# Kernel optimization log

Hardware: AMD Instinct MI355X
Metric: run time of the kernel (lower is better)

Reference implementation:

```python
import jax, jax.numpy as jnp
import numpy as np

NEG_INF = -1e30  # safe -inf surrogate to avoid nan in logsumexp


def _ctc_loss_sum(log_probs, labels, input_lengths, label_lengths):
    # log_probs: (T, N, C) already log-softmaxed; blank = 0
    T, N, C = log_probs.shape
    S = labels.shape[1]
    L = 2 * S + 1  # extended label sequence: blank-interleaved

    # extended labels: [blank, y1, blank, y2, ..., blank]
    ext = jnp.zeros((N, L), dtype=jnp.int32).at[:, 1::2].set(labels.astype(jnp.int32))
    # gather emission log-probs for extended labels: (T, N, L)
    lp_ext = jnp.take_along_axis(log_probs, jnp.broadcast_to(ext[None], (T, N, L)), axis=2)

    # transition from l-2 allowed only for non-blank labels differing from ext[l-2]
    ext_m2 = jnp.pad(ext, ((0, 0), (2, 0)), constant_values=-1)[:, :L]
    allow_skip = (ext != 0) & (ext != ext_m2)  # (N, L)

    # alpha at t=0
    alpha0 = jnp.full((N, L), NEG_INF, dtype=log_probs.dtype)
    alpha0 = alpha0.at[:, 0].set(lp_ext[0, :, 0])
    alpha0 = alpha0.at[:, 1].set(jnp.where(label_lengths > 0, lp_ext[0, :, 1], NEG_INF))

    def step(alpha, t_and_lp):
        t, lp_t = t_and_lp  # lp_t: (N, L)
        a1 = jnp.pad(alpha, ((0, 0), (1, 0)), constant_values=NEG_INF)[:, :L]
        a2 = jnp.pad(alpha, ((0, 0), (2, 0)), constant_values=NEG_INF)[:, :L]
        a2 = jnp.where(allow_skip, a2, NEG_INF)
        m = jnp.maximum(jnp.maximum(alpha, a1), a2)
        lse = m + jnp.log(jnp.exp(alpha - m) + jnp.exp(a1 - m) + jnp.exp(a2 - m))
        new = jnp.where(m > NEG_INF / 2, lse + lp_t, NEG_INF)
        # freeze alpha past each sequence's input length
        alpha = jnp.where((t < input_lengths)[:, None], new, alpha)
        return alpha, None

    alpha, _ = jax.lax.scan(step, alpha0, (jnp.arange(1, T), lp_ext[1:]))

    # log-likelihood = logsumexp(alpha[2*Sl], alpha[2*Sl - 1])
    idx = (2 * label_lengths).astype(jnp.int32)
    a_last = jnp.take_along_axis(alpha, idx[:, None], axis=1)[:, 0]
    a_prev = jnp.take_along_axis(alpha, jnp.maximum(idx - 1, 0)[:, None], axis=1)[:, 0]
    a_prev = jnp.where(label_lengths > 0, a_prev, NEG_INF)
    m = jnp.maximum(a_last, a_prev)
    ll = m + jnp.log(jnp.exp(a_last - m) + jnp.exp(a_prev - m))
    loss = -ll
    # zero_infinity=True: replace infinite losses with 0
    loss = jnp.where(loss < -NEG_INF / 2, loss, 0.0)
    return jnp.sum(loss)


def setup_inputs() -> dict:
    T, N, C, S = 512, 32, 4000, 64
    key = jax.random.key(0)
    k1, k2 = jax.random.split(key)
    inputs = jax.random.normal(k1, (T, N, C), dtype=jnp.float32)
    labels = jax.random.randint(k2, (N, S), 1, C, dtype=jnp.int32)  # exclude blank=0
    input_lengths = jnp.full((N,), T, dtype=jnp.int32)
    label_lengths = jnp.full((N,), S, dtype=jnp.int32)
    return {"inputs": inputs, "labels": labels,
            "input_lengths": input_lengths, "label_lengths": label_lengths}


def reference(inputs, labels, input_lengths, label_lengths):
    log_probs = jax.nn.log_softmax(inputs, axis=2)
    return _ctc_loss_sum(log_probs, labels, input_lengths, label_lengths)
```

## Files before the change

kernel.cpp:

```cpp
#include <hip/hip_runtime.h>

#define LN2 0.6931471805599453f

constexpr int T = 512, N = 32, C = 4000, S = 64;
constexpr int TN   = T * N;
constexpr int ROWF = 68;
constexpr int CT   = 16;
constexpr int NCF  = 16;
constexpr int NCB  = 16;
constexpr int NCG  = 32;

__global__ __launch_bounds__(256) void k_softmax_probs(
    const float* __restrict__ x, const int* __restrict__ labels,
    float* __restrict__ pp, float* __restrict__ ee)
{
    int row  = blockIdx.x * 4 + (threadIdx.x >> 6);
    int lane = threadIdx.x & 63;
    const float*  rp  = x + (size_t)row * C;
    const float4* rp4 = reinterpret_cast<const float4*>(rp);

    float m = -INFINITY, s = 0.f;
    #pragma unroll
    for (int k = 0; k < 15; ++k) {
        float4 v = rp4[lane + 64 * k];
        float mv = fmaxf(fmaxf(v.x, v.y), fmaxf(v.z, v.w));
        float s4 = __expf(v.x - mv) + __expf(v.y - mv) +
                   __expf(v.z - mv) + __expf(v.w - mv);
        float nm = fmaxf(m, mv);
        s = s * __expf(m - nm) + s4 * __expf(mv - nm);
        m = nm;
    }
    if (lane < 40) {
        float4 v = rp4[960 + lane];
        float mv = fmaxf(fmaxf(v.x, v.y), fmaxf(v.z, v.w));
        float s4 = __expf(v.x - mv) + __expf(v.y - mv) +
                   __expf(v.z - mv) + __expf(v.w - mv);
        float nm = fmaxf(m, mv);
        s = s * __expf(m - nm) + s4 * __expf(mv - nm);
        m = nm;
    }
    for (int off = 32; off; off >>= 1) {
        float om = __shfl_xor(m, off), os = __shfl_xor(s, off);
        float nm = fmaxf(m, om);
        s = s * __expf(m - nm) + os * __expf(om - nm);
        m = nm;
    }
    float logZ = m + __logf(s);

    int t = row >> 5, n = row & 31;
    int c  = labels[n * S + lane];
    float zb = rp[0];
    float zl = rp[c];

    float wm = zl;
    for (int off = 32; off; off >>= 1) wm = fmaxf(wm, __shfl_xor(wm, off));
    wm = fmaxf(wm, zb);
    float pm = __expf(wm - logZ);
    int e = (int)(__float_as_uint(pm) >> 23) - 127;

    float* outp = pp + ((size_t)n * T + t) * ROWF;
    outp[1 + lane] = ldexpf(__expf(zl - logZ), -e);
    if (lane == 0) {
        outp[0] = ldexpf(__expf(zb - logZ), -e);
        ee[n * T + t] = (float)e;
    }
}

__device__ __forceinline__ float dpp_shr1_zero(float x) {
    int r = __builtin_amdgcn_update_dpp(0, __float_as_int(x),
                                        0x138 , 0xf, 0xf, false);
    return __int_as_float(r);
}
__device__ __forceinline__ float dpp_shl1_zero(float x) {
    int r = __builtin_amdgcn_update_dpp(0, __float_as_int(x),
                                        0x130 , 0xf, 0xf, false);
    return __int_as_float(r);
}
template <int CTRL>
__device__ __forceinline__ float dpp_max_step(float x) {
    int t = __builtin_amdgcn_update_dpp(__float_as_int(x), __float_as_int(x),
                                        CTRL, 0xf, 0xf, false);
    return fmaxf(x, __int_as_float(t));
}
__device__ __forceinline__ float wave_max_bcast(float x) {
    x = dpp_max_step<0xB1>(x);  x = dpp_max_step<0x4E>(x);
    x = dpp_max_step<0x141>(x); x = dpp_max_step<0x140>(x);
    x = dpp_max_step<0x142>(x); x = dpp_max_step<0x143>(x);
    return __int_as_float(__builtin_amdgcn_readlane(__float_as_int(x), 63));
}

__global__ __launch_bounds__(128) void k_ctc_alpha(
    const float* __restrict__ pp, const float* __restrict__ ee,
    const int* __restrict__ labels,
    const int* __restrict__ input_len, const int* __restrict__ label_len,
    float* __restrict__ out)
{
    __shared__ __align__(16) float ldsF[2][CT][ROWF];
    __shared__ __align__(16) float ldsB[2][CT][ROWF];
    __shared__ float gj[132];
    const int n = blockIdx.x;
    const int wid = threadIdx.x >> 6, lane = threadIdx.x & 63;
    const int Tin = input_len[n], Sl = label_len[n];
    const float* bp = pp + (size_t)n * T * ROWF;
    const bool hot = (Tin == T);

    const int li   = labels[n * S + lane];
    const int lim1 = lane ? labels[n * S + lane - 1] : -1;
    const float skf  = (lane > 0 && li != 0 && li != lim1) ? 1.f : 0.f;
    const float skUf = dpp_shr1_zero(skf);
    const float skk  = skf * skUf;
    const float skD  = dpp_shl1_zero(skf);

    asm volatile("s_waitcnt vmcnt(0)" ::: "memory");
    __builtin_amdgcn_sched_barrier(0);

    float a0 = 0.f, a1 = 0.f, aX = 0.f;
    int SH = 0;

#define ISSUE_F(cc) do {                                                      \
    const float* cp_ = bp + (size_t)(cc) * CT * ROWF;                         \
    if (lane < 17) {                                                          \
        _Pragma("unroll")                                                     \
        for (int d_ = 0; d_ < CT; ++d_)                                       \
            __builtin_amdgcn_global_load_lds(cp_ + (size_t)d_ * ROWF + lane * 4, \
                                             &ldsF[(cc) & 1][d_][0], 16, 0, 0);\
    } } while (0)
#define ISSUE_B(cc) do {                                                      \
    const float* cp_ = bp + (size_t)(496 - 16 * (cc)) * ROWF;                 \
    if (lane < 17) {                                                          \
        _Pragma("unroll")                                                     \
        for (int d_ = 0; d_ < CT; ++d_)                                       \
            __builtin_amdgcn_global_load_lds(cp_ + (size_t)d_ * ROWF + lane * 4, \
                                             &ldsB[(cc) & 1][d_][0], 16, 0, 0);\
    } } while (0)

#define PAIRS(B, D) do {                                                      \
    const float* R0_ = &ldsF[B][D][0];                                        \
    const float* R1_ = &ldsF[B][(D) + 1][0];                                  \
    float cb1 = R0_[0], cl1 = R0_[1 + lane];                                  \
    float cb2 = R1_[0], cl2 = R1_[1 + lane];                                  \
    float clU = dpp_shr1_zero(cl1);                                           \
    float W   = clU * cl2;                                                    \
    float A   = cb1 * cb2;                                                    \
    float B_  = clU * cb2;                                                    \
    float Cc  = A + B_;                                                       \
    float D_  = skUf * B_;                                                    \
    float s1  = cb1 + cl1;                                                    \
    float E   = s1 * cl2;                                                     \
    float F   = cl1 * cl2;                                                    \
    float G   = skf * W;                                                      \
    float H   = fmaf(skf, F + W, cb1 * cl2);                                  \
    float I   = skk * W;                                                      \
    float Y0  = cl1 * cb2;                                                    \
    float Y1  = s1 * cb2;                                                     \
    float Y2  = skf * Y0;                                                     \
    float p1  = dpp_shr1_zero(a1);                                            \
    float p0  = dpp_shr1_zero(a0);                                            \
    float p2  = dpp_shr1_zero(p1);                                            \
    float n0  = fmaf(p0, B_, a0 * A) + fmaf(p2, D_, p1 * Cc);                 \
    float n1  = fmaf(a1, F, a0 * E) + fmaf(p2, I, fmaf(p1, H, p0 * G));       \
    float nX  = fmaf(a1, Y1, aX * A) + fmaf(p1, Y2, a0 * Y0);                 \
    a0 = n0; a1 = n1; aX = nX;                                                \
} while (0)

#define WINDOW4(B, D0) do {                                                   \
    a0 = ldexpf(a0, kA); a1 = ldexpf(a1, kA); aX = ldexpf(aX, kA);            \
    SH += kA;                                                                 \
    float gnow_ = fmaxf(fmaxf(a0, a1), aX);                                   \
    PAIRS(B, D0);                                                             \
    gs = dpp_max_step<0xB1>(gs);  gs = dpp_max_step<0x4E>(gs);                \
    PAIRS(B, (D0) + 2);                                                       \
    gs = dpp_max_step<0x141>(gs); gs = dpp_max_step<0x140>(gs);               \
    PAIRS(B, (D0) + 4);                                                       \
    gs = dpp_max_step<0x142>(gs); gs = dpp_max_step<0x143>(gs);               \
    PAIRS(B, (D0) + 6);                                                       \
    {   unsigned b_ = (unsigned)__builtin_amdgcn_readlane(__float_as_int(gs), 63); \
        int e_ = (int)(b_ >> 23) - 127;                                       \
        kA = (b_ == 0u) ? 0 : (105 - e_ - kA);                                \
    }                                                                         \
    gs = gnow_;                                                               \
} while (0)

#define BSTEPT(B, D) do {                                                     \
    const float* R_ = &ldsB[B][D][0];                                         \
    float cb_ = R_[0], cl_ = R_[1 + lane];                                    \
    float cD_ = dpp_shl1_zero(cl_);                         \
    float d1_ = dpp_shl1_zero(g1);                           \
    float d0s_ = dpp_shl1_zero(g0);                          \
    float d0_ = (lane == 63) ? gX : d0s_;             \
    float cg_ = cl_ * g1;                                                     \
    float ng0 = fmaf(cb_, g0, cg_);                                           \
    float ng1 = fmaf(skD * cD_, d1_, fmaf(cb_, d0_, cg_));                    \
    float ngX = cb_ * gX;                                                     \
    g0 = ng0; g1 = ng1; gX = ngX;                                             \
} while (0)
#define BRENORM do {                                                          \
    float g_ = wave_max_bcast(fmaxf(g0, fmaxf(g1, gX)));                      \
    unsigned b_ = __float_as_uint(g_);                                        \
    int k_ = (b_ == 0u) ? 0 : (100 - ((int)(b_ >> 23) - 127));                \
    g0 = ldexpf(g0, k_); g1 = ldexpf(g1, k_); gX = ldexpf(gX, k_);            \
    SHb += k_;                                                                \
} while (0)

    if (wid == 0) {
        if (hot) {
            int kA = 0; float gs = 0.f;
            ISSUE_F(0); ISSUE_F(1);
            asm volatile("s_waitcnt vmcnt(16)" ::: "memory");
            __builtin_amdgcn_sched_barrier(0);
            a0 = (lane == 0) ? ldsF[0][0][0] : 0.f;
            a1 = (lane == 0 && Sl > 0) ? ldsF[0][0][1] : 0.f;
            {
                float cb = ldsF[0][1][0], cl = ldsF[0][1][1 + lane];
                float p1 = dpp_shr1_zero(a1);
                float n0 = (a0 + p1) * cb;
                float n1 = fmaf(skf, p1, a0 + a1) * cl;
                float nX = (aX + a1) * cb;
                a0 = n0; a1 = n1; aX = nX;
            }
            PAIRS(0, 2); PAIRS(0, 4); PAIRS(0, 6);
            {   float g = wave_max_bcast(fmaxf(fmaxf(a0, a1), aX));
                unsigned b = __float_as_uint(g);
                int k0 = (b == 0u) ? 0 : (105 - ((int)(b >> 23) - 127));
                a0 = ldexpf(a0, k0); a1 = ldexpf(a1, k0); aX = ldexpf(aX, k0);
                SH += k0; kA = 0;
                gs = fmaxf(fmaxf(a0, a1), aX);
            }
            WINDOW4(0, 8);
            __builtin_amdgcn_sched_barrier(0);
            ISSUE_F(2);
            for (int c = 1; c < NCF; ++c) {
                if (c < NCF - 1) { asm volatile("s_waitcnt vmcnt(16)" ::: "memory"); }
                else             { asm volatile("s_waitcnt vmcnt(0)"  ::: "memory"); }
                __builtin_amdgcn_sched_barrier(0);
                int buf = c & 1;
                WINDOW4(buf, 0);
                WINDOW4(buf, 8);
                if (c + 2 < NCF) {
                    __builtin_amdgcn_sched_barrier(0);
                    ISSUE_F(c + 2);
                }
            }
        } else {
#define GSTEP(cc, dd) do {                                                    \
    float cb_ = ldsF[(cc) & 1][dd][0];                                        \
    float cl_ = ldsF[(cc) & 1][dd][1 + lane];                                 \
    float p1_ = dpp_shr1_zero(a1);                                            \
    float na0_ = (a0 + p1_) * cb_;                                            \
    float na1_ = fmaf(skf, p1_, a0 + a1) * cl_;                               \
    float naX_ = (aX + a1) * cb_;                                             \
    int t_ = (cc) * CT + (dd);                                                \
    bool act_ = (unsigned)(t_ - 1) < (unsigned)(Tin - 1);                     \
    a0 = act_ ? na0_ : a0;                                                    \
    a1 = act_ ? na1_ : a1;                                                    \
    aX = act_ ? naX_ : aX;                                                    \
    if (((dd) & 3) == 3) {                                                    \
        float g_ = wave_max_bcast(fmaxf(a0, fmaxf(a1, aX)));                  \
        unsigned b_ = __float_as_uint(g_);                                    \
        int k_ = (b_ == 0u) ? 0 : (100 - ((int)(b_ >> 23) - 127));            \
        a0 = ldexpf(a0, k_); a1 = ldexpf(a1, k_); aX = ldexpf(aX, k_);        \
        SH += k_;                                                             \
    }                                                                         \
} while (0)
            ISSUE_F(0); ISSUE_F(1);
            asm volatile("s_waitcnt vmcnt(16)" ::: "memory");
            __builtin_amdgcn_sched_barrier(0);
            a0 = (lane == 0) ? ldsF[0][0][0] : 0.f;
            a1 = (lane == 0 && Sl > 0) ? ldsF[0][0][1] : 0.f;
            #pragma unroll
            for (int d = 1; d < CT; ++d) GSTEP(0, d);
            __builtin_amdgcn_sched_barrier(0);
            ISSUE_F(2);
            for (int c = 1; c < NCG; ++c) {
                if (c < NCG - 1) { asm volatile("s_waitcnt vmcnt(16)" ::: "memory"); }
                else             { asm volatile("s_waitcnt vmcnt(0)"  ::: "memory"); }
                __builtin_amdgcn_sched_barrier(0);
                #pragma unroll
                for (int d = 0; d < CT; ++d) GSTEP(c, d);
                if (c + 2 < NCG) {
                    __builtin_amdgcn_sched_barrier(0);
                    ISSUE_F(c + 2);
                }
            }
#undef GSTEP
        }
    } else if (hot) {
        float g0 = (lane == Sl) ? 1.f : 0.f;
        float g1 = (Sl > 0 && lane == Sl - 1) ? 1.f : 0.f;
        float gX = (Sl >= S && lane == 63) ? 1.f : 0.f;
        int SHb = 0;

        ISSUE_B(0); ISSUE_B(1);
        for (int c = 0; c < NCB; ++c) {
            if (c < NCB - 1) { asm volatile("s_waitcnt vmcnt(16)" ::: "memory"); }
            else             { asm volatile("s_waitcnt vmcnt(0)"  ::: "memory"); }
            __builtin_amdgcn_sched_barrier(0);
            int buf = c & 1;
            BSTEPT(buf, 15); BSTEPT(buf, 14); BSTEPT(buf, 13); BSTEPT(buf, 12);
            BRENORM;
            BSTEPT(buf, 11); BSTEPT(buf, 10); BSTEPT(buf, 9);  BSTEPT(buf, 8);
            BRENORM;
            BSTEPT(buf, 7);  BSTEPT(buf, 6);  BSTEPT(buf, 5);  BSTEPT(buf, 4);
            BRENORM;
            BSTEPT(buf, 3);  BSTEPT(buf, 2);  BSTEPT(buf, 1);  BSTEPT(buf, 0);
            BRENORM;
            if (c + 2 < NCB) {
                __builtin_amdgcn_sched_barrier(0);
                ISSUE_B(c + 2);
            }
        }
        gj[2 * lane]     = ldexpf(g0, -120);
        gj[2 * lane + 1] = ldexpf(g1, -120);
        if (lane == 63) {
            gj[128] = ldexpf(gX, -120);
            gj[130] = (float)SHb;
        }
    }

    __syncthreads();
    if (wid != 0) return;

    float se = 0.f;
    #pragma unroll
    for (int j = 0; j < 8; ++j) {
        int idx = lane + 64 * j;
        float ev = ee[n * T + idx];
        se += (idx < Tin) ? ev : 0.f;
    }
    for (int off = 32; off; off >>= 1) se += __shfl_xor(se, off);

    if (hot) {
        float term = a0 * gj[2 * lane] + a1 * gj[2 * lane + 1];
        if (lane == 63) term = fmaf(aX, gj[128], term);
        for (int off = 32; off; off >>= 1) term += __shfl_xor(term, off);
        if (lane == 0) {
            float SHb = gj[130];
            float ll2  = log2f(term) - (float)SH - SHb + 120.f + se;
            float loss = -ll2 * LN2;
            if (!(loss < 5e29f)) loss = 0.f;
            atomicAdd(out, loss);
        }
    } else {
        float a_last = (Sl >= S) ? __shfl(aX, 63) : __shfl(a0, Sl);
        float a_prev_raw = __shfl(a1, (Sl > 0) ? (Sl - 1) : 0);
        float a_prev = (Sl > 0) ? a_prev_raw : 0.f;
        if (lane == 0) {
            float sum  = a_last + a_prev;
            float ll2  = log2f(sum) - (float)SH + se;
            float loss = -ll2 * LN2;
            if (!(loss < 5e29f)) loss = 0.f;
            atomicAdd(out, loss);
        }
    }
#undef BRENORM
#undef BSTEPT
#undef WINDOW4
#undef PAIRS
#undef ISSUE_F
#undef ISSUE_B
}

extern "C" void kernel_launch(void* const* d_in, const int* in_sizes, int n_in,
                              void* d_out, int out_size, void* d_ws, size_t ws_size,
                              hipStream_t stream) {
    const float* x       = (const float*)d_in[0];
    const int*   labels  = (const int*)d_in[1];
    const int*   in_len  = (const int*)d_in[2];
    const int*   lab_len = (const int*)d_in[3];
    float* out  = (float*)d_out;
    float* pp   = (float*)d_ws;
    float* ee   = pp + (size_t)TN * ROWF + 256;

    hipMemsetAsync(out, 0, sizeof(float), stream);
    k_softmax_probs<<<TN / 4, 256, 0, stream>>>(x, labels, pp, ee);
    k_ctc_alpha<<<N, 128, 0, stream>>>(pp, ee, labels, in_len, lab_len, out);
}
```

Before: 81.55 us.

## Fuse backward CTC steps into two-step transfer and rebalance forward/backward chunks

The backward beta recursion now advances two timesteps per update by precomposing the two emission rows into a banded two-step transfer matrix. This halves the serial dependent DPP/FMA chain per step pair. The meeting point moves so the forward pass handles 8 chunks and the backward pass 24, balancing the now cheaper backward wave against the forward wave. The final combine switches to double precision and drops the fixed ldexp offset. The cost is more arithmetic per pair and changed rounding behaviour.

```diff
diff --git a/kernel.cpp b/kernel.cpp
--- a/kernel.cpp
+++ b/kernel.cpp
@@ -6,8 +6,8 @@
 constexpr int TN   = T * N;
 constexpr int ROWF = 68;
 constexpr int CT   = 16;
-constexpr int NCF  = 16;
-constexpr int NCB  = 16;
+constexpr int NCF  = 8;
+constexpr int NCB  = 24;
 constexpr int NCG  = 32;
 
 __global__ __launch_bounds__(256) void k_softmax_probs(
@@ -110,6 +110,7 @@
     const float skUf = dpp_shr1_zero(skf);
     const float skk  = skf * skUf;
     const float skD  = dpp_shl1_zero(skf);
+    const float skD2 = dpp_shl1_zero(skD);
 
     asm volatile("s_waitcnt vmcnt(0)" ::: "memory");
     __builtin_amdgcn_sched_barrier(0);
@@ -181,18 +182,33 @@
     gs = gnow_;                                                               \
 } while (0)
 
-#define BSTEPT(B, D) do {                                                     \
-    const float* R_ = &ldsB[B][D][0];                                         \
-    float cb_ = R_[0], cl_ = R_[1 + lane];                                    \
-    float cD_ = dpp_shl1_zero(cl_);                         \
-    float d1_ = dpp_shl1_zero(g1);                           \
-    float d0s_ = dpp_shl1_zero(g0);                          \
-    float d0_ = (lane == 63) ? gX : d0s_;             \
-    float cg_ = cl_ * g1;                                                     \
-    float ng0 = fmaf(cb_, g0, cg_);                                           \
-    float ng1 = fmaf(skD * cD_, d1_, fmaf(cb_, d0_, cg_));                    \
-    float ngX = cb_ * gX;                                                     \
-    g0 = ng0; g1 = ng1; gX = ngX;                                             \
+#define CPAIR(B, D) do {                                                      \
+    const float* Ru_ = &ldsB[B][D][0];                                        \
+    const float* Rv_ = &ldsB[B][(D) + 1][0];                                  \
+    float ub_ = Ru_[0], ul_ = Ru_[1 + lane];                                  \
+    float vb_ = Rv_[0], vl_ = Rv_[1 + lane];                                  \
+    float ulp_ = dpp_shl1_zero(ul_);                                          \
+    float vlp_ = dpp_shl1_zero(vl_);                                          \
+    float vlpp_ = dpp_shl1_zero(vlp_);                                        \
+    float A2_  = ub_ * vb_;                                                   \
+    float uv_  = ul_ * vl_;                                                   \
+    float c00_ = vl_ * (ub_ + ul_);                                           \
+    float c01_ = ul_ * vb_;                                                   \
+    float c02_ = (ul_ * skD) * vlp_;                                          \
+    float d01_ = (ul_ + ub_) * vb_;                                           \
+    float d02_ = vlp_ * fmaf(skD, ul_ + ulp_, ub_);                           \
+    float d03_ = (skD * vb_) * ulp_;                                          \
+    float d04_ = ((skD * skD2) * ulp_) * vlpp_;                               \
+    float g0n1s_ = dpp_shl1_zero(g0);                                         \
+    float g0n1_ = (lane == 63) ? gX : g0n1s_;                                 \
+    float g1n1_ = dpp_shl1_zero(g1);                                          \
+    float g0n2_ = dpp_shl1_zero(g0n1_);                     \
+    float g1n2_ = dpp_shl1_zero(g1n1_);                                       \
+    float n0_ = fmaf(g0, A2_, g1 * c00_) + fmaf(g0n1_, c01_, g1n1_ * c02_);   \
+    float n1_ = fmaf(g1, uv_, g0n1_ * d01_) +                                 \
+                fmaf(g1n1_, d02_, fmaf(g0n2_, d03_, g1n2_ * d04_));           \
+    float nX_ = A2_ * gX;                                                     \
+    g0 = n0_; g1 = n1_; gX = nX_;                                             \
 } while (0)
 #define BRENORM do {                                                          \
     float g_ = wave_max_bcast(fmaxf(g0, fmaxf(g1, gX)));                      \
@@ -296,23 +312,23 @@
             else             { asm volatile("s_waitcnt vmcnt(0)"  ::: "memory"); }
             __builtin_amdgcn_sched_barrier(0);
             int buf = c & 1;
-            BSTEPT(buf, 15); BSTEPT(buf, 14); BSTEPT(buf, 13); BSTEPT(buf, 12);
+            CPAIR(buf, 14); CPAIR(buf, 12);
             BRENORM;
-            BSTEPT(buf, 11); BSTEPT(buf, 10); BSTEPT(buf, 9);  BSTEPT(buf, 8);
+            CPAIR(buf, 10); CPAIR(buf, 8);
             BRENORM;
-            BSTEPT(buf, 7);  BSTEPT(buf, 6);  BSTEPT(buf, 5);  BSTEPT(buf, 4);
+            CPAIR(buf, 6);  CPAIR(buf, 4);
             BRENORM;
-            BSTEPT(buf, 3);  BSTEPT(buf, 2);  BSTEPT(buf, 1);  BSTEPT(buf, 0);
+            CPAIR(buf, 2);  CPAIR(buf, 0);
             BRENORM;
             if (c + 2 < NCB) {
                 __builtin_amdgcn_sched_barrier(0);
                 ISSUE_B(c + 2);
             }
         }
-        gj[2 * lane]     = ldexpf(g0, -120);
-        gj[2 * lane + 1] = ldexpf(g1, -120);
+        gj[2 * lane]     = g0;
+        gj[2 * lane + 1] = g1;
         if (lane == 63) {
-            gj[128] = ldexpf(gX, -120);
+            gj[128] = gX;
             gj[130] = (float)SHb;
         }
     }
@@ -330,13 +346,14 @@
     for (int off = 32; off; off >>= 1) se += __shfl_xor(se, off);
 
     if (hot) {
-        float term = a0 * gj[2 * lane] + a1 * gj[2 * lane + 1];
-        if (lane == 63) term = fmaf(aX, gj[128], term);
+        double term = (double)a0 * (double)gj[2 * lane]
+                    + (double)a1 * (double)gj[2 * lane + 1];
+        if (lane == 63) term += (double)aX * (double)gj[128];
         for (int off = 32; off; off >>= 1) term += __shfl_xor(term, off);
         if (lane == 0) {
-            float SHb = gj[130];
-            float ll2  = log2f(term) - (float)SH - SHb + 120.f + se;
-            float loss = -ll2 * LN2;
+            double SHb = (double)gj[130];
+            double ll2 = log2(term) - (double)SH - SHb + (double)se;
+            float loss = (float)(-ll2 * (double)LN2);
             if (!(loss < 5e29f)) loss = 0.f;
             atomicAdd(out, loss);
         }
@@ -353,7 +370,7 @@
         }
     }
 #undef BRENORM
-#undef BSTEPT
+#undef CPAIR
 #undef WINDOW4
 #undef PAIRS
 #undef ISSUE_F
```

Result: slower. 95.82 us (+17.5%).
